# Kernel tuning notes

Measured on AMD Instinct MI355X. Metric: run time of the kernel, lower is better.

## Reference

```python
import jax, jax.numpy as jnp
import numpy as np

ALIGN_H = 14
ALIGN_W = 14


def setup_inputs() -> dict:
    key = jax.random.key(0)
    k1, k2 = jax.random.split(key)
    feature_map = jax.random.normal(k1, (8, 64, 64, 256), dtype=jnp.float32)
    rois = jax.random.uniform(k2, (8, 128, 4), dtype=jnp.float32)  # [y1,x1,y2,x2] in [0,1] (tf crop_and_resize order)
    return {"feature_map": feature_map, "rois": rois}


def _crop_and_resize(image, boxes, box_indices, crop_h, crop_w):
    """Faithful jax port of tf.image.crop_and_resize (bilinear, extrapolation_value=0).
    image: [B,H,W,C]; boxes: [N,4] normalized [y1,x1,y2,x2]; box_indices: [N] int32.
    Returns [N, crop_h, crop_w, C]. Assumes crop_h, crop_w > 1 (as here: 14x14)."""
    B, H, W, C = image.shape
    y1, x1, y2, x2 = boxes[:, 0], boxes[:, 1], boxes[:, 2], boxes[:, 3]

    i = jnp.arange(crop_h, dtype=image.dtype)
    j = jnp.arange(crop_w, dtype=image.dtype)
    h_scale = (y2 - y1) * (H - 1) / (crop_h - 1)          # [N]
    w_scale = (x2 - x1) * (W - 1) / (crop_w - 1)          # [N]
    in_y = y1[:, None] * (H - 1) + i[None, :] * h_scale[:, None]   # [N, ch]
    in_x = x1[:, None] * (W - 1) + j[None, :] * w_scale[:, None]   # [N, cw]

    valid_y = (in_y >= 0) & (in_y <= H - 1)               # [N, ch]
    valid_x = (in_x >= 0) & (in_x <= W - 1)               # [N, cw]

    top_y = jnp.clip(jnp.floor(in_y), 0, H - 1).astype(jnp.int32)
    bot_y = jnp.clip(jnp.ceil(in_y), 0, H - 1).astype(jnp.int32)
    lft_x = jnp.clip(jnp.floor(in_x), 0, W - 1).astype(jnp.int32)
    rgt_x = jnp.clip(jnp.ceil(in_x), 0, W - 1).astype(jnp.int32)
    y_lerp = (in_y - jnp.floor(in_y))[:, :, None, None]   # [N, ch, 1, 1]
    x_lerp = (in_x - jnp.floor(in_x))[:, None, :, None]   # [N, 1, cw, 1]

    b = box_indices[:, None, None]                        # [N,1,1]
    # gather only the needed pixels -> [N, ch, cw, C]
    tl = image[b, top_y[:, :, None], lft_x[:, None, :], :]
    tr = image[b, top_y[:, :, None], rgt_x[:, None, :], :]
    bl = image[b, bot_y[:, :, None], lft_x[:, None, :], :]
    br = image[b, bot_y[:, :, None], rgt_x[:, None, :], :]

    top = tl + (tr - tl) * x_lerp
    bot = bl + (br - bl) * x_lerp
    out = top + (bot - top) * y_lerp

    valid = (valid_y[:, :, None] & valid_x[:, None, :])[:, :, :, None]
    return jnp.where(valid, out, jnp.zeros((), image.dtype))


def reference(feature_map, rois):
    batch_size, num_rois, _ = rois.shape
    box_indices = jnp.repeat(jnp.arange(batch_size, dtype=jnp.int32), num_rois)
    boxes = rois.reshape(-1, 4)
    return _crop_and_resize(feature_map, boxes, box_indices, ALIGN_H, ALIGN_W)
```

## Files before the change

### kernel.cpp

```cpp
#include <hip/hip_runtime.h>


#define B_   8
#define H_   64
#define W_   64
#define C4_  64
#define NROI 128
#define CH_  14
#define CW_  14
#define PIX_PER_BATCH (NROI * CH_ * CW_)
#define NPIX (B_ * PIX_PER_BATCH)
#define PIXHALVES_PER_BLOCK 8
#define BLOCKS_PER_XCDPHASE (PIX_PER_BATCH / PIXHALVES_PER_BLOCK)
#define BLOCKS_PER_PHASE (BLOCKS_PER_XCDPHASE * 8)
#define BLOCKS_TOTAL (BLOCKS_PER_PHASE * 2)

__global__ __launch_bounds__(256) void roi_crop_resize_kernel(
    const float4* __restrict__ fm,
    const float*  __restrict__ rois,
    float4*       __restrict__ out)
{
    int m     = (int)blockIdx.x;
    int phase = (m >= BLOCKS_PER_PHASE) ? 1 : 0;
    int mm    = m - phase * BLOCKS_PER_PHASE;
    int xcd   = mm & 7;
    int slot  = mm >> 3;

    int batch = phase * 4 + (xcd >> 1);
    int half  = xcd & 1;

    int tid = (int)threadIdx.x;
    int ph  = slot * PIXHALVES_PER_BLOCK + (tid >> 5);
    int cg  = half * 32 + (tid & 31);

    int j = ph % CW_;
    int t = ph / CW_;
    int i = t % CH_;
    int r = t / CH_;
    int n = batch * NROI + r;
    int pix = batch * PIX_PER_BATCH + ph;

    const float* box = rois + n * 4;
    float y1 = box[0], x1 = box[1], y2 = box[2], x2 = box[3];

    const float Hm1 = (float)(H_ - 1);
    const float Wm1 = (float)(W_ - 1);

    float h_scale = (y2 - y1) * Hm1 / (float)(CH_ - 1);
    float w_scale = (x2 - x1) * Wm1 / (float)(CW_ - 1);

    float in_y = y1 * Hm1 + (float)i * h_scale;
    float in_x = x1 * Wm1 + (float)j * w_scale;

    bool valid = (in_y >= 0.0f) & (in_y <= Hm1) & (in_x >= 0.0f) & (in_x <= Wm1);

    float fy = floorf(in_y);
    float fx = floorf(in_x);
    float cy = ceilf(in_y);
    float cx = ceilf(in_x);

    int ty = (int)fminf(fmaxf(fy, 0.0f), Hm1);
    int by = (int)fminf(fmaxf(cy, 0.0f), Hm1);
    int lx = (int)fminf(fmaxf(fx, 0.0f), Wm1);
    int rx = (int)fminf(fmaxf(cx, 0.0f), Wm1);

    float yl = in_y - fy;
    float xl = in_x - fx;

    int rowT = (batch * H_ + ty) * W_;
    int rowB = (batch * H_ + by) * W_;

    float4 tl = fm[(rowT + lx) * C4_ + cg];
    float4 tr = fm[(rowT + rx) * C4_ + cg];
    float4 bl = fm[(rowB + lx) * C4_ + cg];
    float4 br = fm[(rowB + rx) * C4_ + cg];

    float4 o;
    {
        float top, bot;
        top = tl.x + (tr.x - tl.x) * xl;
        bot = bl.x + (br.x - bl.x) * xl;
        o.x = top + (bot - top) * yl;
        top = tl.y + (tr.y - tl.y) * xl;
        bot = bl.y + (br.y - bl.y) * xl;
        o.y = top + (bot - top) * yl;
        top = tl.z + (tr.z - tl.z) * xl;
        bot = bl.z + (br.z - bl.z) * xl;
        o.z = top + (bot - top) * yl;
        top = tl.w + (tr.w - tl.w) * xl;
        bot = bl.w + (br.w - bl.w) * xl;
        o.w = top + (bot - top) * yl;
    }

    if (!valid) { o.x = 0.0f; o.y = 0.0f; o.z = 0.0f; o.w = 0.0f; }

    out[(size_t)pix * C4_ + cg] = o;
}

extern "C" void kernel_launch(void* const* d_in, const int* in_sizes, int n_in,
                              void* d_out, int out_size, void* d_ws, size_t ws_size,
                              hipStream_t stream) {
    const float4* fm   = (const float4*)d_in[0];
    const float*  rois = (const float*)d_in[1];
    float4*       out  = (float4*)d_out;

    roi_crop_resize_kernel<<<BLOCKS_TOTAL, 256, 0, stream>>>(fm, rois, out);
}
```

Before: 249.1 us.

## Process two output pixels per thread and drop XCD-aware batch mapping

Each wave of 64 threads now covers a full 256-channel pixel, and each thread computes two output pixels (j0 and j0+7), issuing eight independent float4 loads. This halves the number of blocks and raises memory-level parallelism per thread. It also removes the old block-to-XCD mapping that pinned each batch's feature map to a particular XCD's L2, so cache locality for feature-map reuse may get worse.

```diff
diff --git a/kernel.cpp b/kernel.cpp
--- a/kernel.cpp
+++ b/kernel.cpp
@@ -8,37 +8,25 @@
 #define NROI 128
 #define CH_  14
 #define CW_  14
-#define PIX_PER_BATCH (NROI * CH_ * CW_)
-#define NPIX (B_ * PIX_PER_BATCH)
-#define PIXHALVES_PER_BLOCK 8
-#define BLOCKS_PER_XCDPHASE (PIX_PER_BATCH / PIXHALVES_PER_BLOCK)
-#define BLOCKS_PER_PHASE (BLOCKS_PER_XCDPHASE * 8)
-#define BLOCKS_TOTAL (BLOCKS_PER_PHASE * 2)
+#define TASKS_PER_ROI (CH_ * 7)
+#define NTASKS (B_ * NROI * TASKS_PER_ROI)
+#define WAVES_PER_BLOCK 4
+#define BLOCKS_TOTAL (NTASKS / WAVES_PER_BLOCK)
 
 __global__ __launch_bounds__(256) void roi_crop_resize_kernel(
     const float4* __restrict__ fm,
     const float*  __restrict__ rois,
     float4*       __restrict__ out)
 {
-    int m     = (int)blockIdx.x;
-    int phase = (m >= BLOCKS_PER_PHASE) ? 1 : 0;
-    int mm    = m - phase * BLOCKS_PER_PHASE;
-    int xcd   = mm & 7;
-    int slot  = mm >> 3;
+    int tid = (int)threadIdx.x;
+    int wt  = (int)blockIdx.x * WAVES_PER_BLOCK + (tid >> 6);
+    int cg  = tid & 63;
 
-    int batch = phase * 4 + (xcd >> 1);
-    int half  = xcd & 1;
-
-    int tid = (int)threadIdx.x;
-    int ph  = slot * PIXHALVES_PER_BLOCK + (tid >> 5);
-    int cg  = half * 32 + (tid & 31);
-
-    int j = ph % CW_;
-    int t = ph / CW_;
-    int i = t % CH_;
-    int r = t / CH_;
-    int n = batch * NROI + r;
-    int pix = batch * PIX_PER_BATCH + ph;
+    int n  = wt / TASKS_PER_ROI;
+    int t  = wt - n * TASKS_PER_ROI;
+    int i  = t / 7;
+    int j0 = t - i * 7;
+    int b  = n >> 7;
 
     const float* box = rois + n * 4;
     float y1 = box[0], x1 = box[1], y2 = box[2], x2 = box[3];
@@ -50,51 +38,79 @@
     float w_scale = (x2 - x1) * Wm1 / (float)(CW_ - 1);
 
     float in_y = y1 * Hm1 + (float)i * h_scale;
-    float in_x = x1 * Wm1 + (float)j * w_scale;
+    bool  vy   = (in_y >= 0.0f) & (in_y <= Hm1);
+    float fy   = floorf(in_y);
+    float cy   = ceilf(in_y);
+    int   ty   = (int)fminf(fmaxf(fy, 0.0f), Hm1);
+    int   by   = (int)fminf(fmaxf(cy, 0.0f), Hm1);
+    float yl   = in_y - fy;
+    int rowT   = (b * H_ + ty) * W_;
+    int rowB   = (b * H_ + by) * W_;
 
-    bool valid = (in_y >= 0.0f) & (in_y <= Hm1) & (in_x >= 0.0f) & (in_x <= Wm1);
+    float in_xa = x1 * Wm1 + (float)j0 * w_scale;
+    bool  vxa   = (in_xa >= 0.0f) & (in_xa <= Wm1);
+    float fxa   = floorf(in_xa);
+    float cxa   = ceilf(in_xa);
+    int   lxa   = (int)fminf(fmaxf(fxa, 0.0f), Wm1);
+    int   rxa   = (int)fminf(fmaxf(cxa, 0.0f), Wm1);
+    float xla   = in_xa - fxa;
 
-    float fy = floorf(in_y);
-    float fx = floorf(in_x);
-    float cy = ceilf(in_y);
-    float cx = ceilf(in_x);
+    float in_xb = x1 * Wm1 + (float)(j0 + 7) * w_scale;
+    bool  vxb   = (in_xb >= 0.0f) & (in_xb <= Wm1);
+    float fxb   = floorf(in_xb);
+    float cxb   = ceilf(in_xb);
+    int   lxb   = (int)fminf(fmaxf(fxb, 0.0f), Wm1);
+    int   rxb   = (int)fminf(fmaxf(cxb, 0.0f), Wm1);
+    float xlb   = in_xb - fxb;
 
-    int ty = (int)fminf(fmaxf(fy, 0.0f), Hm1);
-    int by = (int)fminf(fmaxf(cy, 0.0f), Hm1);
-    int lx = (int)fminf(fmaxf(fx, 0.0f), Wm1);
-    int rx = (int)fminf(fmaxf(cx, 0.0f), Wm1);
+    float4 aTL = fm[(rowT + lxa) * C4_ + cg];
+    float4 aTR = fm[(rowT + rxa) * C4_ + cg];
+    float4 aBL = fm[(rowB + lxa) * C4_ + cg];
+    float4 aBR = fm[(rowB + rxa) * C4_ + cg];
+    float4 bTL = fm[(rowT + lxb) * C4_ + cg];
+    float4 bTR = fm[(rowT + rxb) * C4_ + cg];
+    float4 bBL = fm[(rowB + lxb) * C4_ + cg];
+    float4 bBR = fm[(rowB + rxb) * C4_ + cg];
 
-    float yl = in_y - fy;
-    float xl = in_x - fx;
+    bool va = vy & vxa;
+    bool vb = vy & vxb;
 
-    int rowT = (batch * H_ + ty) * W_;
-    int rowB = (batch * H_ + by) * W_;
-
-    float4 tl = fm[(rowT + lx) * C4_ + cg];
-    float4 tr = fm[(rowT + rx) * C4_ + cg];
-    float4 bl = fm[(rowB + lx) * C4_ + cg];
-    float4 br = fm[(rowB + rx) * C4_ + cg];
-
-    float4 o;
+    float4 oa, ob;
     {
         float top, bot;
-        top = tl.x + (tr.x - tl.x) * xl;
-        bot = bl.x + (br.x - bl.x) * xl;
-        o.x = top + (bot - top) * yl;
-        top = tl.y + (tr.y - tl.y) * xl;
-        bot = bl.y + (br.y - bl.y) * xl;
-        o.y = top + (bot - top) * yl;
-        top = tl.z + (tr.z - tl.z) * xl;
-        bot = bl.z + (br.z - bl.z) * xl;
-        o.z = top + (bot - top) * yl;
-        top = tl.w + (tr.w - tl.w) * xl;
-        bot = bl.w + (br.w - bl.w) * xl;
-        o.w = top + (bot - top) * yl;
+        top = aTL.x + (aTR.x - aTL.x) * xla;
+        bot = aBL.x + (aBR.x - aBL.x) * xla;
+        oa.x = top + (bot - top) * yl;
+        top = aTL.y + (aTR.y - aTL.y) * xla;
+        bot = aBL.y + (aBR.y - aBL.y) * xla;
+        oa.y = top + (bot - top) * yl;
+        top = aTL.z + (aTR.z - aTL.z) * xla;
+        bot = aBL.z + (aBR.z - aBL.z) * xla;
+        oa.z = top + (bot - top) * yl;
+        top = aTL.w + (aTR.w - aTL.w) * xla;
+        bot = aBL.w + (aBR.w - aBL.w) * xla;
+        oa.w = top + (bot - top) * yl;
+
+        top = bTL.x + (bTR.x - bTL.x) * xlb;
+        bot = bBL.x + (bBR.x - bBL.x) * xlb;
+        ob.x = top + (bot - top) * yl;
+        top = bTL.y + (bTR.y - bTL.y) * xlb;
+        bot = bBL.y + (bBR.y - bBL.y) * xlb;
+        ob.y = top + (bot - top) * yl;
+        top = bTL.z + (bTR.z - bTL.z) * xlb;
+        bot = bBL.z + (bBR.z - bBL.z) * xlb;
+        ob.z = top + (bot - top) * yl;
+        top = bTL.w + (bTR.w - bTL.w) * xlb;
+        bot = bBL.w + (bBR.w - bBL.w) * xlb;
+        ob.w = top + (bot - top) * yl;
     }
 
-    if (!valid) { o.x = 0.0f; o.y = 0.0f; o.z = 0.0f; o.w = 0.0f; }
+    if (!va) { oa.x = 0.0f; oa.y = 0.0f; oa.z = 0.0f; oa.w = 0.0f; }
+    if (!vb) { ob.x = 0.0f; ob.y = 0.0f; ob.z = 0.0f; ob.w = 0.0f; }
 
-    out[(size_t)pix * C4_ + cg] = o;
+    size_t basepix = ((size_t)n * CH_ + i) * CW_;
+    out[(basepix + j0)     * C4_ + cg] = oa;
+    out[(basepix + j0 + 7) * C4_ + cg] = ob;
 }
 
 extern "C" void kernel_launch(void* const* d_in, const int* in_sizes, int n_in,
```

After: 247.6 us (median of 2 runs). About the same (-0.6%).
